# Kernel optimization log

Measured on AMD Instinct MI355X. Metric: run time of the kernel, lower is better.

Reference implementation:

```python
import jax, jax.numpy as jnp
import numpy as np

K = 8  # hardcoded knn_point(8, ...) in the original module


def setup_inputs() -> dict:
    key = jax.random.key(0)
    k1, k2, k3 = jax.random.split(key, 3)
    B, N, S, C = 8, 8192, 2048, 256
    return {
        "xyz": jax.random.normal(k1, (B, 3, N), dtype=jnp.float32),
        "sparse_xyz": jax.random.normal(k2, (B, 3, S), dtype=jnp.float32),
        "sparse_feat": jax.random.normal(k3, (B, C, S), dtype=jnp.float32),
    }


def reference(xyz, sparse_xyz, sparse_feat):
    # xyz: [B,3,N] dense query points; sparse_xyz: [B,3,S]; sparse_feat: [B,C,S]
    B, _, N = xyz.shape
    x = jnp.transpose(xyz, (0, 2, 1))          # [B,N,3]
    sx = jnp.transpose(sparse_xyz, (0, 2, 1))  # [B,S,3]
    sf = jnp.transpose(sparse_feat, (0, 2, 1)) # [B,S,C]

    sqr = (jnp.sum(x * x, axis=-1)[:, :, None]
           + jnp.sum(sx * sx, axis=-1)[:, None, :]
           - 2.0 * jnp.einsum('bnc,bsc->bns', x, sx))

    # K nearest neighbors (smallest distance) -> indices [B,N,K]
    _, idx = jax.lax.top_k(-sqr, K)

    bidx = jnp.arange(B)[:, None, None]
    g_xyz = sx[bidx, idx]                      # gather neighbor coords [B,N,K,3]
    diff = g_xyz - x[:, :, None, :]
    dist = jnp.maximum(jnp.linalg.norm(diff, axis=3), 1e-10)  # [B,N,K]

    inv = 1.0 / dist
    weight = inv / jnp.sum(inv, axis=2, keepdims=True)        # [B,N,K]

    g_feat = sf[bidx, idx]                     # gather neighbor feats [B,N,K,C]
    dense = jnp.sum(weight[..., None] * g_feat, axis=2)       # [B,N,C]
    return jnp.transpose(dense, (0, 2, 1))     # [B,C,N]
```

## Files before the change

kernel.cpp:

```cpp
#include <hip/hip_runtime.h>
#include <hip/hip_fp16.h>

#define BB 8
#define NN 8192
#define SS 2048
#define CC 256
#define KNN 8
#define TOPM 10
#define NLIST 4
#define QPB 64
#define MSTRIDE 41
#define FSTR 12

#define UMIN(a, b) __builtin_elementwise_min(a, b)
#define UMAX(a, b) __builtin_elementwise_max(a, b)
#define UMIN3(a, b, c) UMIN(UMIN(a, b), c)

typedef short bf16x8_t __attribute__((ext_vector_type(8)));
typedef float f32x4_t __attribute__((ext_vector_type(4)));

__device__ __forceinline__ unsigned pack_h2(float a, float b) {
    __half2 h = __halves2half2(__float2half_rn(a), __float2half_rn(b));
    return *reinterpret_cast<unsigned*>(&h);
}
__device__ __forceinline__ float2 unpack_h2(unsigned u) {
    __half2 h = *reinterpret_cast<__half2*>(&u);
    return __half22float2(h);
}

__device__ __forceinline__ unsigned short f2bf(float f) {
    unsigned u = __float_as_uint(f);
    u += 0x7FFFu + ((u >> 16) & 1u);
    return (unsigned short)(u >> 16);
}
__device__ __forceinline__ float bf2f(unsigned short h) {
    return __uint_as_float((unsigned)h << 16);
}

__device__ __forceinline__ void ins2(unsigned k1[TOPM], unsigned ca, unsigned cb) {
    unsigned lo = UMIN(ca, cb), hi = UMAX(ca, cb);
#pragma unroll
    for (int j = TOPM - 1; j >= 2; --j)
        k1[j] = UMIN3(k1[j], UMAX(k1[j - 1], lo), UMAX(k1[j - 2], hi));
    k1[1] = UMIN3(k1[1], UMAX(k1[0], lo), hi);
    k1[0] = UMIN(k1[0], lo);
}

__device__ __forceinline__ void ins_step(unsigned k1[TOPM], f32x4_t d, unsigned sbase) {
    unsigned c0 = (__float_as_uint(d[0]) & 0xFFFFF800u) | sbase;
    unsigned c1 = (__float_as_uint(d[1]) & 0xFFFFF800u) | (sbase + 1u);
    unsigned c2 = (__float_as_uint(d[2]) & 0xFFFFF800u) | (sbase + 2u);
    unsigned c3 = (__float_as_uint(d[3]) & 0xFFFFF800u) | (sbase + 3u);
    ins2(k1, c0, c1);
    ins2(k1, c2, c3);
}

__global__ __launch_bounds__(256) void prep_kernel(
    const float* __restrict__ sxyz,
    unsigned short* __restrict__ gt)
{
    const int b = blockIdx.x;
    const int tid = threadIdx.x;
    const float* sb = sxyz + (long)b * 3 * SS;
    unsigned short* gb = gt + (long)b * 2 * SS * 8;
#pragma unroll
    for (int i = 0; i < SS / 256; ++i) {
        int s = i * 256 + tid;
        float px = sb[s], py = sb[SS + s], pz = sb[2 * SS + s];
        unsigned short xh = f2bf(px); unsigned short xl = f2bf(px - bf2f(xh));
        unsigned short yh = f2bf(py); unsigned short yl = f2bf(py - bf2f(yh));
        unsigned short zh = f2bf(pz); unsigned short zl = f2bf(pz - bf2f(zh));
        float pn = fmaf(px, px, fmaf(py, py, pz * pz));
        unsigned short nh = f2bf(pn); unsigned short nl = f2bf(pn - bf2f(nh));
        const unsigned ONE = 0x3F80u;
        uint4 t0 = make_uint4((unsigned)xh | ((unsigned)xl << 16),
                              (unsigned)xh | ((unsigned)yh << 16),
                              (unsigned)yl | ((unsigned)yh << 16),
                              (unsigned)zh | ((unsigned)zl << 16));
        uint4 t1 = make_uint4((unsigned)zh | ((unsigned)nh << 16),
                              (unsigned)nl | (ONE << 16),
                              ONE, 0u);
        *(uint4*)&gb[(long)s * 8] = t0;
        *(uint4*)&gb[((long)SS + s) * 8] = t1;
    }
}

__global__ __launch_bounds__(256, 4) void knn_kernel(
    const float* __restrict__ xyz,
    const float* __restrict__ sxyz,
    const unsigned short* __restrict__ gt,
    unsigned* __restrict__ out_pk)
{
    __shared__ unsigned mbuf[QPB * MSTRIDE];

    const int b    = blockIdx.x >> 7;
    const int q0   = (blockIdx.x & 127) * QPB;
    const int tid  = threadIdx.x;
    const int wave = tid >> 6;
    const int lane = tid & 63;
    const int g    = lane >> 4;
    const int qi   = lane & 15;

    const float* sb = sxyz + (long)b * 3 * SS;
    const float* xb = xyz + (long)b * 3 * NN;

    const int nq = q0 + wave * 16 + qi;
    const float qx = xb[nq], qy = xb[NN + nq], qz = xb[2 * NN + nq];

    bf16x8_t qf = (bf16x8_t)0;
    {
        unsigned short xh = f2bf(qx); float xhf = bf2f(xh);
        unsigned short yh = f2bf(qy); float yhf = bf2f(yh);
        unsigned short zh = f2bf(qz); float zhf = bf2f(zh);
        unsigned short xh2 = f2bf(-2.f * xhf), xl2 = f2bf(-2.f * (qx - xhf));
        unsigned short yh2 = f2bf(-2.f * yhf), yl2 = f2bf(-2.f * (qy - yhf));
        unsigned short zh2 = f2bf(-2.f * zhf), zl2 = f2bf(-2.f * (qz - zhf));
        float qn = fmaf(qx, qx, fmaf(qy, qy, qz * qz)) + 0.0625f;
        unsigned short nh = f2bf(qn); unsigned short nl = f2bf(qn - bf2f(nh));
        const short ONE = (short)0x3F80;
        if (g == 0) {
            qf[0] = (short)xh2; qf[1] = (short)xh2; qf[2] = (short)xl2;
            qf[3] = (short)yh2; qf[4] = (short)yh2; qf[5] = (short)yl2;
            qf[6] = (short)zh2; qf[7] = (short)zh2;
        } else if (g == 1) {
            qf[0] = (short)zl2; qf[1] = ONE; qf[2] = ONE;
            qf[3] = (short)nh;  qf[4] = (short)nl;
        }
    }

    const unsigned short* abase =
        gt + (long)b * 2 * SS * 8 + (long)(g & 1) * SS * 8 + qi * 8;

    unsigned k1[TOPM];
#pragma unroll
    for (int j = 0; j < TOPM; ++j) k1[j] = 0xFFFFFFFFu;

    const f32x4_t zacc = {0.f, 0.f, 0.f, 0.f};
    const unsigned ib4 = (unsigned)(g * 4);

    bf16x8_t af = *(const bf16x8_t*)abase; abase += 128;
    f32x4_t dc = __builtin_amdgcn_mfma_f32_16x16x32_bf16(af, qf, zacc, 0, 0, 0);

#pragma unroll 2
    for (int step = 0; step < 127; ++step) {
        bf16x8_t an = *(const bf16x8_t*)abase; abase += 128;
        f32x4_t dn = __builtin_amdgcn_mfma_f32_16x16x32_bf16(an, qf, zacc, 0, 0, 0);
        ins_step(k1, dc, ib4 + (unsigned)(step * 16));
        dc = dn;
    }
    ins_step(k1, dc, ib4 + (unsigned)(127 * 16));

    {
        unsigned* m1 = &mbuf[(wave * 16 + qi) * MSTRIDE + g * TOPM];
#pragma unroll
        for (int j = 0; j < TOPM; ++j) m1[j] = k1[j];
    }
    __syncthreads();

    if (tid < QPB) {
        const int n2 = q0 + tid;
        const double dqx = (double)xb[n2], dqy = (double)xb[NN + n2], dqz = (double)xb[2 * NN + n2];
        const unsigned* ml = &mbuf[tid * MSTRIDE];

        unsigned long long top[KNN];
#pragma unroll
        for (int j = 0; j < KNN; ++j) top[j] = ~0ull;

#pragma unroll 4
        for (int j = 0; j < NLIST * TOPM; ++j) {
            unsigned key = ml[j];
            int s = key & 0x7FF;
            float px = sb[s], py = sb[SS + s], pz = sb[2 * SS + s];
            double ex = (double)px - dqx;
            double ey = (double)py - dqy;
            double ez = (double)pz - dqz;
            double dd = ex * ex + ey * ey + ez * ez;
            unsigned long long c =
                (((unsigned long long)__double_as_longlong(dd)) & ~0x7FFull) | (unsigned long long)s;
#pragma unroll
            for (int jj = KNN - 1; jj >= 1; --jj)
                top[jj] = UMIN(UMAX(top[jj - 1], c), top[jj]);
            top[0] = UMIN(top[0], c);
        }

        const float fqx = xb[n2], fqy = xb[NN + n2], fqz = xb[2 * NN + n2];
        int   id[KNN];
        float inv[KNN];
        float ssum = 0.f;
#pragma unroll
        for (int k = 0; k < KNN; ++k) {
            id[k] = (int)(top[k] & 0x7FFull);
            float px = sb[id[k]], py = sb[SS + id[k]], pz = sb[2 * SS + id[k]];
            float dx = px - fqx, dy = py - fqy, dz = pz - fqz;
            float dv = sqrtf(dx * dx + dy * dy + dz * dz);
            dv = fmaxf(dv, 1e-10f);
            inv[k] = 1.0f / dv;
            ssum += inv[k];
        }
        const float rs = 1.0f / ssum;
        const long base = ((long)b * NN + n2) * KNN;
#pragma unroll
        for (int k = 0; k < KNN; ++k) {
            unsigned hw = (unsigned)__half_as_ushort(__float2half_rn(inv[k] * rs));
            out_pk[base + k] = (hw << 16) | (unsigned)id[k];
        }
    }
}

__global__ __launch_bounds__(256, 2) void accum_kernel(
    const float*    __restrict__ sf,
    const unsigned* __restrict__ pk,
    float* __restrict__ out)
{
    __shared__ unsigned short feat[SS * FSTR];

    const int blk  = blockIdx.x;
    const int b    = blk >> 6;
    const int ct   = (blk >> 1) & 31;
    const int half = blk & 1;
    const int t    = threadIdx.x;
    const int c0   = ct * 8;

    const float* sfb = sf + ((long)b * CC + c0) * SS;
#pragma unroll
    for (int i = 0; i < SS / 256; ++i) {
        int s = i * 256 + t;
        float f[8];
#pragma unroll
        for (int c = 0; c < 8; ++c) f[c] = sfb[(long)c * SS + s];
        uint2 w0 = make_uint2(pack_h2(f[0], f[1]), pack_h2(f[2], f[3]));
        uint2 w1 = make_uint2(pack_h2(f[4], f[5]), pack_h2(f[6], f[7]));
        *(uint2*)&feat[s * FSTR]     = w0;
        *(uint2*)&feat[s * FSTR + 4] = w1;
    }
    __syncthreads();

    const unsigned* pkb = pk + ((long)b * NN + half * 4096) * KNN;
    float* outb = out + ((long)b * CC + c0) * NN + half * 4096;

    for (int it = 0; it < 4096 / 256; ++it) {
        const int nrel = it * 256 + t;
        const uint4 pa = *(const uint4*)(pkb + (long)nrel * KNN);
        const uint4 pb = *(const uint4*)(pkb + (long)nrel * KNN + 4);
        const unsigned pks[8] = {pa.x, pa.y, pa.z, pa.w, pb.x, pb.y, pb.z, pb.w};

        float acc[8];
#pragma unroll
        for (int c = 0; c < 8; ++c) acc[c] = 0.f;

#pragma unroll
        for (int k = 0; k < KNN; ++k) {
            const unsigned p = pks[k];
            const int id = p & 0x7FF;
            const float w = __half2float(__ushort_as_half((unsigned short)(p >> 16)));
            const unsigned short* fp = &feat[id * FSTR];
            uint2 A = *(const uint2*)fp;
            uint2 B = *(const uint2*)(fp + 4);
            float2 f0 = unpack_h2(A.x), f1 = unpack_h2(A.y);
            float2 f2 = unpack_h2(B.x), f3 = unpack_h2(B.y);
            acc[0] = fmaf(w, f0.x, acc[0]);
            acc[1] = fmaf(w, f0.y, acc[1]);
            acc[2] = fmaf(w, f1.x, acc[2]);
            acc[3] = fmaf(w, f1.y, acc[3]);
            acc[4] = fmaf(w, f2.x, acc[4]);
            acc[5] = fmaf(w, f2.y, acc[5]);
            acc[6] = fmaf(w, f3.x, acc[6]);
            acc[7] = fmaf(w, f3.y, acc[7]);
        }

#pragma unroll
        for (int c = 0; c < 8; ++c)
            outb[(long)c * NN + nrel] = acc[c];
    }
}

extern "C" void kernel_launch(void* const* d_in, const int* in_sizes, int n_in,
                              void* d_out, int out_size, void* d_ws, size_t ws_size,
                              hipStream_t stream) {
    const float* xyz  = (const float*)d_in[0];
    const float* sxyz = (const float*)d_in[1];
    const float* sf   = (const float*)d_in[2];
    float* out = (float*)d_out;

    unsigned* pkbuf = (unsigned*)d_ws;
    unsigned short* gtile = (unsigned short*)((char*)d_ws + (size_t)BB * NN * KNN * 4);

    prep_kernel<<<dim3(BB), dim3(256), 0, stream>>>(sxyz, gtile);
    knn_kernel<<<dim3(BB * NN / QPB), dim3(256), 0, stream>>>(xyz, sxyz, gtile, pkbuf);
    accum_kernel<<<dim3(BB * 32 * 2), dim3(256), 0, stream>>>(sf, pkbuf, out);
}
```

Before: 175.6 us.

## Restructure knn MFMA loop prefetch and split accum into quarter blocks with smaller LDS

The knn inner loop now prefetches two tile loads ahead and issues two MFMAs per iteration, replacing the one-deep software pipeline. The accum kernel drops the padded 12-short feature stride in favour of a dense 8-short layout read with single 128-bit LDS loads. It also splits each batch/channel tile across four blocks instead of two, raises launch bounds to 4 blocks per CU, and prefetches the next neighbor-index packet. The aim is more parallelism and latency hiding in accum. The trade-off is possible LDS bank conflicts from the unpadded stride and extra redundant feature staging, since each block now loads the full feature slice for fewer queries.

```diff
diff --git a/kernel.cpp b/kernel.cpp
--- a/kernel.cpp
+++ b/kernel.cpp
@@ -10,7 +10,6 @@
 #define NLIST 4
 #define QPB 64
 #define MSTRIDE 41
-#define FSTR 12
 
 #define UMIN(a, b) __builtin_elementwise_min(a, b)
 #define UMAX(a, b) __builtin_elementwise_max(a, b)
@@ -128,7 +127,7 @@
         }
     }
 
-    const unsigned short* abase =
+    const unsigned short* ap =
         gt + (long)b * 2 * SS * 8 + (long)(g & 1) * SS * 8 + qi * 8;
 
     unsigned k1[TOPM];
@@ -138,17 +137,24 @@
     const f32x4_t zacc = {0.f, 0.f, 0.f, 0.f};
     const unsigned ib4 = (unsigned)(g * 4);
 
-    bf16x8_t af = *(const bf16x8_t*)abase; abase += 128;
-    f32x4_t dc = __builtin_amdgcn_mfma_f32_16x16x32_bf16(af, qf, zacc, 0, 0, 0);
-
-#pragma unroll 2
-    for (int step = 0; step < 127; ++step) {
-        bf16x8_t an = *(const bf16x8_t*)abase; abase += 128;
-        f32x4_t dn = __builtin_amdgcn_mfma_f32_16x16x32_bf16(an, qf, zacc, 0, 0, 0);
-        ins_step(k1, dc, ib4 + (unsigned)(step * 16));
-        dc = dn;
-    }
-    ins_step(k1, dc, ib4 + (unsigned)(127 * 16));
+    bf16x8_t a0 = *(const bf16x8_t*)ap; ap += 128;
+    bf16x8_t a1 = *(const bf16x8_t*)ap; ap += 128;
+
+    for (int step = 0; step < 126; step += 2) {
+        bf16x8_t a2 = *(const bf16x8_t*)ap; ap += 128;
+        bf16x8_t a3 = *(const bf16x8_t*)ap; ap += 128;
+        f32x4_t d0 = __builtin_amdgcn_mfma_f32_16x16x32_bf16(a0, qf, zacc, 0, 0, 0);
+        ins_step(k1, d0, ib4 + (unsigned)(step * 16));
+        f32x4_t d1 = __builtin_amdgcn_mfma_f32_16x16x32_bf16(a1, qf, zacc, 0, 0, 0);
+        ins_step(k1, d1, ib4 + (unsigned)((step + 1) * 16));
+        a0 = a2; a1 = a3;
+    }
+    {
+        f32x4_t d0 = __builtin_amdgcn_mfma_f32_16x16x32_bf16(a0, qf, zacc, 0, 0, 0);
+        ins_step(k1, d0, ib4 + (unsigned)(126 * 16));
+        f32x4_t d1 = __builtin_amdgcn_mfma_f32_16x16x32_bf16(a1, qf, zacc, 0, 0, 0);
+        ins_step(k1, d1, ib4 + (unsigned)(127 * 16));
+    }
 
     {
         unsigned* m1 = &mbuf[(wave * 16 + qi) * MSTRIDE + g * TOPM];
@@ -207,19 +213,19 @@
     }
 }
 
-__global__ __launch_bounds__(256, 2) void accum_kernel(
+__global__ __launch_bounds__(256, 4) void accum_kernel(
     const float*    __restrict__ sf,
     const unsigned* __restrict__ pk,
     float* __restrict__ out)
 {
-    __shared__ unsigned short feat[SS * FSTR];
-
-    const int blk  = blockIdx.x;
-    const int b    = blk >> 6;
-    const int ct   = (blk >> 1) & 31;
-    const int half = blk & 1;
-    const int t    = threadIdx.x;
-    const int c0   = ct * 8;
+    __shared__ unsigned short feat[SS * 8];
+
+    const int blk = blockIdx.x;
+    const int b   = blk >> 7;
+    const int ct  = (blk >> 2) & 31;
+    const int qtr = blk & 3;
+    const int t   = threadIdx.x;
+    const int c0  = ct * 8;
 
     const float* sfb = sf + ((long)b * CC + c0) * SS;
 #pragma unroll
@@ -228,20 +234,25 @@
         float f[8];
 #pragma unroll
         for (int c = 0; c < 8; ++c) f[c] = sfb[(long)c * SS + s];
-        uint2 w0 = make_uint2(pack_h2(f[0], f[1]), pack_h2(f[2], f[3]));
-        uint2 w1 = make_uint2(pack_h2(f[4], f[5]), pack_h2(f[6], f[7]));
-        *(uint2*)&feat[s * FSTR]     = w0;
-        *(uint2*)&feat[s * FSTR + 4] = w1;
+        *(uint4*)&feat[s * 8] = make_uint4(pack_h2(f[0], f[1]), pack_h2(f[2], f[3]),
+                                           pack_h2(f[4], f[5]), pack_h2(f[6], f[7]));
     }
     __syncthreads();
 
-    const unsigned* pkb = pk + ((long)b * NN + half * 4096) * KNN;
-    float* outb = out + ((long)b * CC + c0) * NN + half * 4096;
-
-    for (int it = 0; it < 4096 / 256; ++it) {
-        const int nrel = it * 256 + t;
-        const uint4 pa = *(const uint4*)(pkb + (long)nrel * KNN);
-        const uint4 pb = *(const uint4*)(pkb + (long)nrel * KNN + 4);
+    const unsigned* pkb = pk + ((long)b * NN + qtr * 2048) * KNN;
+    const uint4* pkq = (const uint4*)pkb;
+    float* outb = out + ((long)b * CC + c0) * NN + qtr * 2048;
+
+    int nrel = t;
+    uint4 pa = pkq[2 * nrel], pb = pkq[2 * nrel + 1];
+
+#pragma unroll
+    for (int it = 0; it < 2048 / 256; ++it) {
+        uint4 na, nb;
+        if (it < 2048 / 256 - 1) {
+            na = pkq[2 * (nrel + 256)];
+            nb = pkq[2 * (nrel + 256) + 1];
+        }
         const unsigned pks[8] = {pa.x, pa.y, pa.z, pa.w, pb.x, pb.y, pb.z, pb.w};
 
         float acc[8];
@@ -253,11 +264,9 @@
             const unsigned p = pks[k];
             const int id = p & 0x7FF;
             const float w = __half2float(__ushort_as_half((unsigned short)(p >> 16)));
-            const unsigned short* fp = &feat[id * FSTR];
-            uint2 A = *(const uint2*)fp;
-            uint2 B = *(const uint2*)(fp + 4);
-            float2 f0 = unpack_h2(A.x), f1 = unpack_h2(A.y);
-            float2 f2 = unpack_h2(B.x), f3 = unpack_h2(B.y);
+            const uint4 F = *(const uint4*)&feat[id * 8];
+            float2 f0 = unpack_h2(F.x), f1 = unpack_h2(F.y);
+            float2 f2 = unpack_h2(F.z), f3 = unpack_h2(F.w);
             acc[0] = fmaf(w, f0.x, acc[0]);
             acc[1] = fmaf(w, f0.y, acc[1]);
             acc[2] = fmaf(w, f1.x, acc[2]);
@@ -271,6 +280,8 @@
 #pragma unroll
         for (int c = 0; c < 8; ++c)
             outb[(long)c * NN + nrel] = acc[c];
+
+        if (it < 2048 / 256 - 1) { pa = na; pb = nb; nrel += 256; }
     }
 }
 
@@ -287,5 +298,5 @@
 
     prep_kernel<<<dim3(BB), dim3(256), 0, stream>>>(sxyz, gtile);
     knn_kernel<<<dim3(BB * NN / QPB), dim3(256), 0, stream>>>(xyz, sxyz, gtile, pkbuf);
-    accum_kernel<<<dim3(BB * 32 * 2), dim3(256), 0, stream>>>(sf, pkbuf, out);
-}
+    accum_kernel<<<dim3(BB * 32 * 4), dim3(256), 0, stream>>>(sf, pkbuf, out);
+}
```

After: 178.5 us. About the same (+1.6%).
